# Optimization experiments

Measured on AMD Instinct MI355X. Metric: run time of the kernel, lower is better.

Reference implementation:

```python
import jax, jax.numpy as jnp
import numpy as np

B, L, H = 1024, 11, 128          # batch, seq_len-1 observations, cde_hidden_dim
VF, IF = 512, 256                # v_f_len, i_f_len
C = H + 1                        # control channels = time + reduced features
SUBSTEPS = 4                     # fixed RK4 substeps per eval interval (stand-in for solver step control)


def setup_inputs() -> dict:
    key = jax.random.key(0)
    ks = jax.random.split(key, 12)
    rn = lambda k, shape, s: jax.random.normal(k, shape, jnp.float32) * s
    F = VF + IF
    inp = {
        'fv': rn(ks[0], (B, L, VF), 1.0),
        'fi': rn(ks[1], (B, L, IF), 1.0),
        # strictly increasing timestamps
        'ts': jnp.cumsum(jax.random.uniform(ks[2], (B, L + 1), jnp.float32) * 0.1 + 0.01, axis=1),
        'w_red': rn(ks[3], (F, H), F ** -0.5), 'b_red': jnp.zeros((H,), jnp.float32),
        'w_init': rn(ks[4], (C, H), C ** -0.5), 'b_init': jnp.zeros((H,), jnp.float32),
        'w_h1': rn(ks[5], (H, H), H ** -0.5), 'b_h1': jnp.zeros((H,), jnp.float32),
        'w_h2': rn(ks[6], (H, H), H ** -0.5), 'b_h2': jnp.zeros((H,), jnp.float32),
        'w_out': rn(ks[7], (H, H * C), H ** -0.5), 'b_out': jnp.zeros((H * C,), jnp.float32),
        'w_r1': rn(ks[8], (H, 128), H ** -0.5), 'b_r1': jnp.zeros((128,), jnp.float32),
        'w_r2': rn(ks[9], (128, 6), 128 ** -0.5), 'b_r2': jnp.zeros((6,), jnp.float32),
    }
    return inp


def reference(fv, fi, ts, w_red, b_red, w_init, b_init, w_h1, b_h1, w_h2, b_h2,
              w_out, b_out, w_r1, b_r1, w_r2, b_r2):
    # fuse ('cat') + reduction_net
    fused = jnp.concatenate([fv, fi], axis=-1) @ w_red + b_red            # [B,L,H]
    tsd = (ts - ts[:, :1])[:, 1:, None]                                   # [B,L,1]
    x = jnp.concatenate([tsd, fused], axis=-1)                            # [B,L,C] control path; knots at t=0..L-1
    z0 = x[:, 0] @ w_init + b_init                                        # initial hidden state, [B,H]

    def field(z):                                                         # CDEFunc: [B,H] -> [B,H,C]
        h1 = jax.nn.relu(z @ w_h1 + b_h1)
        h2 = jax.nn.relu(h1 @ w_h2 + b_h2)
        return jnp.tanh(h2 @ w_out + b_out).reshape(-1, H, C)

    def dXdt(t):                                                          # piecewise-linear interpolation derivative
        idx = jnp.clip(jnp.floor(t).astype(jnp.int32), 0, L - 2)
        return x[:, idx + 1] - x[:, idx]                                  # [B,C]

    def vf(t, z):                                                         # dz/dt = f(z) @ dX/dt
        return jnp.einsum('bhc,bc->bh', field(z), dXdt(t))

    eval_times = jnp.linspace(0.1, 1.0, 10, dtype=jnp.float32)
    hstep = (eval_times[1] - eval_times[0]) / SUBSTEPS

    def rk4(z, t):
        k1 = vf(t, z)
        k2 = vf(t + hstep / 2, z + hstep / 2 * k1)
        k3 = vf(t + hstep / 2, z + hstep / 2 * k2)
        k4 = vf(t + hstep, z + hstep * k3)
        return z + hstep / 6 * (k1 + 2 * k2 + 2 * k3 + k4)

    def interval(z, t0):
        def body(zc, j):
            return rk4(zc, t0 + j * hstep), None
        z2, _ = jax.lax.scan(body, z, jnp.arange(SUBSTEPS, dtype=jnp.float32))
        return z2, z2

    _, zs = jax.lax.scan(interval, z0, eval_times[:-1])                   # [9,B,H]
    h_T = jnp.concatenate([z0[None], zs], axis=0).transpose(1, 0, 2)      # [B,10,H]

    a = h_T @ w_r1 + b_r1
    a = jnp.where(a > 0, a, 0.1 * a)                                      # LeakyReLU(0.1)
    poses = a @ w_r2 + b_r2                                               # [B,10,6]
    return poses, h_T[:, -1, :]
```

## Files before the change

### kernel.cpp

```cpp
#include <hip/hip_runtime.h>
#include <stdint.h>

typedef float   f32x4 __attribute__((ext_vector_type(4)));
typedef float   f32x2 __attribute__((ext_vector_type(2)));
typedef int     i32x4 __attribute__((ext_vector_type(4)));
typedef int     i32x2 __attribute__((ext_vector_type(2)));
typedef __bf16  bf16x8 __attribute__((ext_vector_type(8)));

#define DEV __device__ __forceinline__

DEV uint16_t f2bf(float f){
  uint32_t u = __float_as_uint(f);
  u += 0x7fffu + ((u >> 16) & 1u);
  return (uint16_t)(u >> 16);
}
DEV uint32_t pkbf(float lo, float hi){
  uint32_t r;
  asm("v_cvt_pk_bf16_f32 %0, %1, %2" : "=v"(r) : "v"(lo), "v"(hi));
  return r;
}
DEV uint32_t aoff(uint32_t row, uint32_t q){ return (row << 8) + (q ^ ((row & 7u) << 4)); }

DEV f32x4 MFMA(bf16x8 a, bf16x8 b, f32x4 c){
  return __builtin_amdgcn_mfma_f32_16x16x32_bf16(a, b, c, 0, 0, 0);
}

DEV uint64_t ld_ic64(const void* p){
  return __hip_atomic_load((const uint64_t*)p, __ATOMIC_RELAXED, __HIP_MEMORY_SCOPE_AGENT);
}
DEV uint32_t ld_ic32(const void* p){
  return __hip_atomic_load((const uint32_t*)p, __ATOMIC_RELAXED, __HIP_MEMORY_SCOPE_AGENT);
}
DEV void st_ic32(void* p, uint32_t v){
  __hip_atomic_store((uint32_t*)p, v, __ATOMIC_RELAXED, __HIP_MEMORY_SCOPE_AGENT);
}

DEV void bar_arrive(uint32_t* bar, uint32_t ep, int grp){
  uint32_t a = __hip_atomic_fetch_add(bar + grp*32, 1u, __ATOMIC_RELAXED, __HIP_MEMORY_SCOPE_AGENT);
  if (a == 32u*ep - 1u){
    uint32_t r = __hip_atomic_fetch_add(bar + 256, 1u, __ATOMIC_RELAXED, __HIP_MEMORY_SCOPE_AGENT);
    if (r == 8u*ep - 1u)
      __hip_atomic_store(bar + 288, ep, __ATOMIC_RELAXED, __HIP_MEMORY_SCOPE_AGENT);
  }
}
DEV void bar_wait(uint32_t* bar, uint32_t ep){
  int spins = 0;
  while (__hip_atomic_load(bar + 288, __ATOMIC_RELAXED, __HIP_MEMORY_SCOPE_AGENT) < ep){
    __builtin_amdgcn_s_sleep(1);
    if (++spins > (1 << 17)) break;
  }
  asm volatile("" ::: "memory");
}

__global__ __launch_bounds__(256) void pose_convT(const float* __restrict__ src,
    uint16_t* __restrict__ dst, int N, int MOD, int CB, float scale)
{
  __shared__ float tile[32][256];
  int bk = blockIdx.x & 3, bn = blockIdx.x >> 2;
  int k0 = bk * 32, n0 = bn * 256;
  int t = threadIdx.x;
  for (int r = 0; r < 32; r++){
    int n = n0 + t;
    tile[r][t] = (n < N) ? src[(size_t)(k0 + r) * N + n] : 0.f;
  }
  __syncthreads();
  int n = n0 + t;
  if (n < N){
    int c = n % MOD, h = n / MOD;
    #pragma unroll
    for (int o = 0; o < 4; o++){
      uint32_t w0 = (uint32_t)f2bf(tile[o*8+0][t]*scale) | ((uint32_t)f2bf(tile[o*8+1][t]*scale) << 16);
      uint32_t w1 = (uint32_t)f2bf(tile[o*8+2][t]*scale) | ((uint32_t)f2bf(tile[o*8+3][t]*scale) << 16);
      uint32_t w2 = (uint32_t)f2bf(tile[o*8+4][t]*scale) | ((uint32_t)f2bf(tile[o*8+5][t]*scale) << 16);
      uint32_t w3 = (uint32_t)f2bf(tile[o*8+6][t]*scale) | ((uint32_t)f2bf(tile[o*8+7][t]*scale) << 16);
      i32x4 val = { (int)w0, (int)w1, (int)w2, (int)w3 };
      uint32_t byte = (uint32_t)c * (uint32_t)CB + aoff((uint32_t)h, (uint32_t)(k0 + o*8) * 2);
      *(i32x4*)((char*)dst + byte) = val;
    }
  }
}

__global__ __launch_bounds__(256) void pose_misc(const float* __restrict__ b_out,
    const float* __restrict__ ts, float* __restrict__ bo_c, float* __restrict__ d0g)
{
  int i = blockIdx.x * 256 + threadIdx.x;
  if (i < 16512){
    int c = i % 129, h = i / 129;
    bo_c[c*128 + h] = b_out[i] * 2.8853900817779268f;
  }
  if (i < 1024) d0g[i] = ts[i*12 + 2] - ts[i*12 + 1];
}

__global__ __launch_bounds__(256) void pose_fused(
    const float* __restrict__ fv, const float* __restrict__ fi,
    const float* __restrict__ w_red, const float* __restrict__ b_red,
    float* __restrict__ F0, float* __restrict__ d0g)
{
  __shared__ float pk[128][16];
  __shared__ float res[16][128];
  const int b0 = blockIdx.x * 8;
  const int t = threadIdx.x;
  const int h = t & 127, sg = t >> 7;
  float acc[8] = {0.f,0.f,0.f,0.f,0.f,0.f,0.f,0.f};
  for (int p = 0; p < 6; p++){
    __syncthreads();
    { const int s  = t >> 4;
      const int ch = (t & 15) * 8;
      const int b  = b0 + (s & 7);
      const int ll = s >> 3;
      const int kb = p*128 + ch;
      const float* src = (kb < 512) ? (fv + ((size_t)b*11 + ll)*512 + kb)
                                    : (fi + ((size_t)b*11 + ll)*256 + (kb - 512));
      float v[8];
      #pragma unroll
      for (int j = 0; j < 8; j++) v[j] = src[j];
      #pragma unroll
      for (int j = 0; j < 8; j++) pk[ch + j][s] = v[j];
    }
    __syncthreads();
    #pragma unroll 4
    for (int kk = 0; kk < 128; kk++){
      const float wv = w_red[(size_t)(p*128 + kk)*128 + h];
      f32x4 v0 = *(const f32x4*)&pk[kk][sg*8];
      f32x4 v1 = *(const f32x4*)&pk[kk][sg*8 + 4];
      acc[0] += v0.x*wv; acc[1] += v0.y*wv; acc[2] += v0.z*wv; acc[3] += v0.w*wv;
      acc[4] += v1.x*wv; acc[5] += v1.y*wv; acc[6] += v1.z*wv; acc[7] += v1.w*wv;
    }
  }
  __syncthreads();
  const float br = b_red[h];
  #pragma unroll
  for (int si = 0; si < 8; si++) res[sg*8 + si][h] = acc[si] + br;
  __syncthreads();
  if (sg == 0){
    #pragma unroll
    for (int si = 0; si < 8; si++){
      const int b = b0 + si;
      const float f0 = res[si][h];
      const float f1 = res[8 + si][h];
      F0[(size_t)b*128 + h] = f0;
      d0g[(size_t)(1 + h)*1024 + b] = f1 - f0;
    }
  }
}

__global__ __launch_bounds__(512) void pose_init(
    const float* __restrict__ F0, const float* __restrict__ ts,
    const float* __restrict__ w_init, const float* __restrict__ b_init,
    const float* __restrict__ d0g,
    float* __restrict__ z_base, uint16_t* __restrict__ zbuf,
    float* __restrict__ hT, float* __restrict__ S)
{
  __shared__ float Ft[128][64];
  const int b0 = blockIdx.x * 64;
  const int t = threadIdx.x;
  { const int b = t >> 3, ch = (t & 7)*16;
    #pragma unroll
    for (int j = 0; j < 16; j++) Ft[ch + j][b] = F0[(size_t)(b0 + b)*128 + ch + j];
  }
  __syncthreads();
  const int h = t & 127, rg = t >> 7;
  float acc[16];
  const float w0 = w_init[h], bi = b_init[h];
  #pragma unroll
  for (int r = 0; r < 16; r++){
    const int b = b0 + rg*16 + r;
    acc[r] = (ts[b*12 + 1] - ts[b*12 + 0]) * w0 + bi;
  }
  #pragma unroll 2
  for (int j = 0; j < 128; j++){
    const float wv = w_init[(j + 1)*128 + h];
    const float* pr = &Ft[j][rg*16];
    #pragma unroll
    for (int q = 0; q < 4; q++){
      f32x4 v = *(const f32x4*)(pr + q*4);
      acc[q*4+0] += v.x*wv; acc[q*4+1] += v.y*wv; acc[q*4+2] += v.z*wv; acc[q*4+3] += v.w*wv;
    }
  }
  #pragma unroll
  for (int r = 0; r < 16; r++){
    const int b = b0 + rg*16 + r;
    const float z = acc[r];
    z_base[(size_t)b*128 + h] = z;
    hT[(size_t)b*1280 + h] = z;
    uint32_t byte = (uint32_t)(b >> 6) * 16384u + aoff((uint32_t)(b & 63), (uint32_t)h*2);
    *(uint16_t*)((char*)zbuf + byte) = f2bf(z);
  }
  if (t < 64){
    const int b = b0 + t;
    float s = 0.f;
    for (int c = 0; c < 129; c++) s += d0g[(size_t)c*1024 + b];
    S[b] = s;
  }
}

__global__ __launch_bounds__(512) void pose_persist(
    const uint16_t* __restrict__ Wt, const uint16_t* __restrict__ w1t,
    const uint16_t* __restrict__ w2t,
    const float* __restrict__ b1, const float* __restrict__ b2,
    const float* __restrict__ bo_c, const float* __restrict__ d0g,
    const float* __restrict__ Sv,
    uint16_t* __restrict__ zbuf, float* __restrict__ partials,
    const float* __restrict__ z_base,
    float* __restrict__ hT, uint32_t* __restrict__ bar)
{
  __shared__ uint16_t Yb[16384];
  __shared__ uint16_t Buf0[16384], Buf1[16384];
  __shared__ uint16_t H1[8192], H2[8192];
  __shared__ float    ztr[8][64];

  const int t   = threadIdx.x;
  const int blk = blockIdx.x;
  const int grp = blk & 7;
  const int mi  = blk >> 4;
  const int ci  = (blk & 7)*2 + ((blk >> 3) & 1);
  const int nc  = (ci == 15) ? 9 : 8;
  const int cbase = ci * 8;
  const int l  = t & 63, w = t >> 6;
  const int hh = w >> 2, bq = w & 3;
  const int l15 = l & 15, l4 = l >> 4;
  const int col16 = bq*16 + l15;
  const int bg = mi*64 + col16;

  const int h0B = (blk & 15) * 8;
  const int hB = h0B + (t >> 6), bB = mi*64 + (t & 63);
  const float HS = 0x1.999996p-6f;
  const float C2 = HS * 0.5f, C6 = HS / 6.f;
  float zb = z_base[(size_t)bB*128 + hB];
  float av = 0.f;
  const float Sb = Sv[bB];
  const char* zsl = (const char*)zbuf + (size_t)mi*16384;

  i32x4 Ra[4];
  auto ldst = [&](const void* g, i32x4* r){
    const i32x4* s = (const i32x4*)g;
    #pragma unroll
    for (int i = 0; i < 4; i++) r[i] = s[t + 512*i];
  };
  auto wrst = [&](uint16_t* lds, const i32x4* r){
    i32x4* d = (i32x4*)lds;
    #pragma unroll
    for (int i = 0; i < 4; i++) d[t + 512*i] = r[i];
  };
  auto chain_core = [&](const uint16_t* Wl, const bf16x8 (&bfr)[4], const float* bias, uint16_t* Dl){
    #pragma unroll
    for (int rt = 0; rt < 4; rt++){
      const int row = hh*64 + rt*16 + l15;
      bf16x8 afr[4];
      #pragma unroll
      for (int kb = 0; kb < 4; kb++)
        afr[kb] = *(const bf16x8*)((const char*)Wl + aoff((uint32_t)row, kb*64 + l4*16));
      const int h0 = hh*64 + rt*16 + l4*4;
      const f32x4 bias4 = *(const f32x4*)(bias + h0);
      f32x4 acc = {0.f,0.f,0.f,0.f};
      #pragma unroll
      for (int kb = 0; kb < 4; kb++) acc = MFMA(afr[kb], bfr[kb], acc);
      const float r0 = fmaxf(acc.x + bias4.x, 0.f);
      const float r1 = fmaxf(acc.y + bias4.y, 0.f);
      const float r2 = fmaxf(acc.z + bias4.z, 0.f);
      const float r3 = fmaxf(acc.w + bias4.w, 0.f);
      i32x2 pv = { (int)pkbf(r0, r1), (int)pkbf(r2, r3) };
      *(i32x2*)((char*)Dl + aoff((uint32_t)col16, (uint32_t)h0*2)) = pv;
    }
  };
  auto ld_bfr_lds = [&](const uint16_t* Bl, bf16x8 (&bfr)[4]){
    #pragma unroll
    for (int kb = 0; kb < 4; kb++)
      bfr[kb] = *(const bf16x8*)((const char*)Bl + aoff((uint32_t)col16, kb*64 + l4*16));
  };

  { i32x4 R0[4], R1[4], R2[4];
    ldst(w1t, R1); ldst(w2t, R2);
    ldst((const char*)Wt + (size_t)cbase*32768, R0);
    ldst((const char*)Wt + (size_t)(cbase + 1)*32768, Ra);
    wrst(Buf0, R1); wrst(Yb, R2); wrst(Buf1, R0);
  }
  __syncthreads();

  #pragma unroll 1
  for (int e = 0; e < 144; e++){
    bf16x8 bz[4];
    #pragma unroll
    for (int kb = 0; kb < 4; kb++){
      const char* a = zsl + aoff((uint32_t)col16, kb*64 + l4*16);
      union { uint64_t q[2]; bf16x8 v; } u;
      u.q[0] = ld_ic64(a);
      u.q[1] = ld_ic64(a + 8);
      bz[kb] = u.v;
    }
    chain_core(Buf0, bz, b1, H1);
    __syncthreads();
    { bf16x8 bh1[4];
      ld_bfr_lds(H1, bh1);
      chain_core(Yb, bh1, b2, H2);
    }
    __syncthreads();
    wrst(Buf0, Ra);

    bf16x8 bfr[4];
    ld_bfr_lds(H2, bfr);

    f32x4 out[4];
    const f32x4 Z4 = {0.f,0.f,0.f,0.f};
    #pragma unroll
    for (int rt = 0; rt < 4; rt++) out[rt] = Z4;

    for (int k = 0; k < nc; k++){
      const int c = cbase + k;
      const uint16_t* Wl = (k & 1) ? Buf0 : Buf1;
      if (k + 2 < nc) ldst((const char*)Wt + (size_t)(cbase + k + 2)*32768, Ra);
      const float d0 = d0g[(size_t)c*1024 + bg];
      #pragma unroll
      for (int rt = 0; rt < 4; rt++){
        const int row = hh*64 + rt*16 + l15;
        bf16x8 afr[4];
        #pragma unroll
        for (int kb = 0; kb < 4; kb++)
          afr[kb] = *(const bf16x8*)((const char*)Wl + aoff((uint32_t)row, kb*64 + l4*16));
        const int h0 = hh*64 + rt*16 + l4*4;
        const f32x4 bo4 = *(const f32x4*)(bo_c + c*128 + h0);
        f32x4 acc = {0.f,0.f,0.f,0.f};
        #pragma unroll
        for (int kb = 0; kb < 4; kb++) acc = MFMA(afr[kb], bfr[kb], acc);
        f32x4 rr;
        rr.x = __builtin_amdgcn_rcpf(__builtin_amdgcn_exp2f(acc.x + bo4.x) + 1.f);
        rr.y = __builtin_amdgcn_rcpf(__builtin_amdgcn_exp2f(acc.y + bo4.y) + 1.f);
        rr.z = __builtin_amdgcn_rcpf(__builtin_amdgcn_exp2f(acc.z + bo4.z) + 1.f);
        rr.w = __builtin_amdgcn_rcpf(__builtin_amdgcn_exp2f(acc.w + bo4.w) + 1.f);
        out[rt] += rr * d0;
      }
      __syncthreads();
      if (k + 2 < nc) wrst((k & 1) ? Buf0 : Buf1, Ra);
    }

    #pragma unroll
    for (int rt = 0; rt < 4; rt++){
      const int h0 = hh*64 + rt*16 + l4*4;
      #pragma unroll
      for (int j = 0; j < 4; j++){
        union { float f; uint32_t u; } v; v.f = out[rt][j];
        st_ic32(&partials[((size_t)ci*128 + h0 + j)*1024 + bg], v.u);
      }
    }
    __syncthreads();
    if (t == 0) bar_arrive(bar, (uint32_t)(2*e + 1), grp);

    if (e < 143){
      i32x4 R0[4], R1[4];
      ldst(w1t, R1);
      ldst((const char*)Wt + (size_t)cbase*32768, R0);
      ldst((const char*)Wt + (size_t)(cbase + 1)*32768, Ra);
      wrst(Buf0, R1); wrst(Buf1, R0);
    }
    if (t == 0) bar_wait(bar, (uint32_t)(2*e + 1));
    __syncthreads();

    {
      float s = 0.f;
      #pragma unroll
      for (int sl = 0; sl < 16; sl++){
        union { uint32_t u; float f; } v;
        v.u = ld_ic32(&partials[((size_t)sl*128 + hB)*1024 + bB]);
        s += v.f;
      }
      const float kk = Sb - 2.f*s;
      const int st = e & 3;
      float ze;
      if (st == 0){      av = kk;        ze = zb + C2*kk; }
      else if (st == 1){ av += 2.f*kk;   ze = zb + C2*kk; }
      else if (st == 2){ av += 2.f*kk;   ze = zb + HS*kk; }
      else {             zb += C6*(av + kk); ze = zb; }
      ztr[t >> 6][t & 63] = ze;
    }
    __syncthreads();
    if (t < 256){
      const int r = t >> 2, pp = t & 3;
      const uint32_t pv = pkbf(ztr[2*pp][r], ztr[2*pp + 1][r]);
      st_ic32((char*)zbuf + (size_t)mi*16384 + aoff((uint32_t)r, (uint32_t)(h0B + 2*pp)*2), pv);
    }
    if ((e & 15) == 15){
      const int r = t >> 3, hl = t & 7;
      hT[(size_t)(mi*64 + r)*1280 + (size_t)((e >> 4) + 1)*128 + h0B + hl] = ztr[hl][r];
    }
    __syncthreads();
    if (e < 143){
      if (t == 0){
        bar_arrive(bar, (uint32_t)(2*e + 2), grp);
        bar_wait(bar, (uint32_t)(2*e + 2));
      }
      __syncthreads();
    }
  }
}

__global__ __launch_bounds__(256) void pose_readout(
    const float* __restrict__ hT, const float* __restrict__ w_r1, const float* __restrict__ b_r1,
    const float* __restrict__ w_r2, const float* __restrict__ b_r2,
    float* __restrict__ out_poses, float* __restrict__ out_z)
{
  if (blockIdx.x >= 320){
    const int cb = blockIdx.x - 320;
    const int base = cb*2048 + threadIdx.x*4;
    #pragma unroll
    for (int p = 0; p < 2; p++){
      const int i = base + p*1024;
      const int b = i >> 7, h = i & 127;
      *(f32x4*)(out_z + i) = *(const f32x4*)(hT + (size_t)b*1280 + 1152 + h);
    }
    return;
  }
  __shared__ float htl[128][32];
  __shared__ float al[32][128];
  const int r0 = blockIdx.x * 32;
  const int t = threadIdx.x;
  { const int row = t >> 3, ch = (t & 7)*16;
    #pragma unroll
    for (int j = 0; j < 16; j++)
      htl[ch + j][row] = hT[(size_t)(r0 + row)*128 + ch + j];
  }
  __syncthreads();
  const int j = t & 127, rg = t >> 7;
  float a[16];
  const float bj = b_r1[j];
  #pragma unroll
  for (int r = 0; r < 16; r++) a[r] = bj;
  #pragma unroll 2
  for (int kk = 0; kk < 128; kk++){
    const float wv = w_r1[(size_t)kk*128 + j];
    const float* pr = &htl[kk][rg*16];
    #pragma unroll
    for (int q = 0; q < 4; q++){
      f32x4 v = *(const f32x4*)(pr + q*4);
      a[q*4+0] += v.x*wv; a[q*4+1] += v.y*wv; a[q*4+2] += v.z*wv; a[q*4+3] += v.w*wv;
    }
  }
  #pragma unroll
  for (int r = 0; r < 16; r++){
    float v = a[r];
    al[rg*16 + r][j] = (v > 0.f) ? v : 0.1f*v;
  }
  __syncthreads();
  if (t < 192){
    const int row = t / 6, p = t % 6;
    float s = b_r2[p];
    const float* ar = al[row];
    #pragma unroll 4
    for (int jj = 0; jj < 128; jj++) s += ar[jj] * w_r2[jj*6 + p];
    out_poses[(size_t)(r0 + row)*6 + p] = s;
  }
}

extern "C" void kernel_launch(void* const* d_in, const int* in_sizes, int n_in,
                              void* d_out, int out_size, void* d_ws, size_t ws_size,
                              hipStream_t stream)
{
  (void)in_sizes; (void)n_in; (void)out_size; (void)ws_size;
  const float* fv    = (const float*)d_in[0];
  const float* fi    = (const float*)d_in[1];
  const float* ts    = (const float*)d_in[2];
  const float* w_red = (const float*)d_in[3];
  const float* b_red = (const float*)d_in[4];
  const float* w_init= (const float*)d_in[5];
  const float* b_init= (const float*)d_in[6];
  const float* w_h1  = (const float*)d_in[7];
  const float* b_h1  = (const float*)d_in[8];
  const float* w_h2  = (const float*)d_in[9];
  const float* b_h2  = (const float*)d_in[10];
  const float* w_out = (const float*)d_in[11];
  const float* b_out = (const float*)d_in[12];
  const float* w_r1  = (const float*)d_in[13];
  const float* b_r1  = (const float*)d_in[14];
  const float* w_r2  = (const float*)d_in[15];
  const float* b_r2  = (const float*)d_in[16];

  char* p = (char*)d_ws;
  auto take = [&](size_t n){ char* r = p; p += (n + 255) & ~(size_t)255; return r; };
  uint32_t* bar   = (uint32_t*)take(4096);
  uint16_t* Wt    = (uint16_t*)take((size_t)129*32768);
  uint16_t* w1t   = (uint16_t*)take(32768);
  uint16_t* w2t   = (uint16_t*)take(32768);
  float* bo_c     = (float*)take((size_t)129*128*4);
  float* d0g      = (float*)take((size_t)129*1024*4);
  float* Sv       = (float*)take(1024*4);
  float* F0       = (float*)take((size_t)1024*128*4);
  float* z_base   = (float*)take((size_t)1024*128*4);
  uint16_t* zbuf  = (uint16_t*)take((size_t)16*16384);
  float* hT       = (float*)take((size_t)1024*10*128*4);
  float* partials = (float*)take((size_t)16*128*1024*4);

  float* out_poses = (float*)d_out;
  float* out_z     = (float*)d_out + 61440;

  const float SC = 2.8853900817779268f;

  hipMemsetAsync(bar, 0, 4096, stream);
  pose_convT<<<4,   256, 0, stream>>>(w_h1,  w1t, 128,   1,   0,     1.0f);
  pose_convT<<<4,   256, 0, stream>>>(w_h2,  w2t, 128,   1,   0,     1.0f);
  pose_convT<<<260, 256, 0, stream>>>(w_out, Wt,  16512, 129, 32768, SC);
  pose_misc <<<65,  256, 0, stream>>>(b_out, ts, bo_c, d0g);
  pose_fused<<<128, 256, 0, stream>>>(fv, fi, w_red, b_red, F0, d0g);
  pose_init <<<16,  512, 0, stream>>>(F0, ts, w_init, b_init, d0g, z_base, zbuf, hT, Sv);

  pose_persist<<<256, 512, 0, stream>>>(Wt, w1t, w2t, b_h1, b_h2, bo_c, d0g, Sv,
                                        zbuf, partials, z_base, hT, bar);

  pose_readout<<<384, 256, 0, stream>>>(hT, w_r1, b_r1, w_r2, b_r2, out_poses, out_z);
}
```

Baseline: 2.849 ms.

## Repartition persistent CDE kernel by hidden slice to keep W_out resident in LDS

The persistent kernel now splits work as 8 batch tiles by 32 hidden-output slices. Each block keeps its full 128KB slice of the output weight resident in LDS instead of streaming control-channel chunks from global memory every step. The cross-block reduction through a global partials buffer and one of the two grid barriers per step are removed, since each block now reduces over all channels locally. z is double-buffered in global memory in an MFMA fragment layout. The cost is that the small h1/h2 MLP is recomputed redundantly in every hidden-slice block, and LDS use rises to about 160KB.

```diff
diff --git a/kernel.cpp b/kernel.cpp
--- a/kernel.cpp
+++ b/kernel.cpp
@@ -24,15 +24,13 @@
 DEV f32x4 MFMA(bf16x8 a, bf16x8 b, f32x4 c){
   return __builtin_amdgcn_mfma_f32_16x16x32_bf16(a, b, c, 0, 0, 0);
 }
+DEV bf16x8 as_bf(i32x4 v){ union { i32x4 i; bf16x8 b; } u; u.i = v; return u.b; }
 
 DEV uint64_t ld_ic64(const void* p){
   return __hip_atomic_load((const uint64_t*)p, __ATOMIC_RELAXED, __HIP_MEMORY_SCOPE_AGENT);
 }
-DEV uint32_t ld_ic32(const void* p){
-  return __hip_atomic_load((const uint32_t*)p, __ATOMIC_RELAXED, __HIP_MEMORY_SCOPE_AGENT);
-}
-DEV void st_ic32(void* p, uint32_t v){
-  __hip_atomic_store((uint32_t*)p, v, __ATOMIC_RELAXED, __HIP_MEMORY_SCOPE_AGENT);
+DEV void st_ic64(void* p, uint64_t v){
+  __hip_atomic_store((uint64_t*)p, v, __ATOMIC_RELAXED, __HIP_MEMORY_SCOPE_AGENT);
 }
 
 DEV void bar_arrive(uint32_t* bar, uint32_t ep, int grp){
@@ -47,54 +45,84 @@
   int spins = 0;
   while (__hip_atomic_load(bar + 288, __ATOMIC_RELAXED, __HIP_MEMORY_SCOPE_AGENT) < ep){
     __builtin_amdgcn_s_sleep(1);
-    if (++spins > (1 << 17)) break;
+    if (++spins > (1 << 20)) break;
   }
   asm volatile("" ::: "memory");
 }
 
-__global__ __launch_bounds__(256) void pose_convT(const float* __restrict__ src,
-    uint16_t* __restrict__ dst, int N, int MOD, int CB, float scale)
+__global__ __launch_bounds__(256) void pose_convW(const float* __restrict__ src,
+    uint16_t* __restrict__ Wg, uint16_t* __restrict__ w0f)
 {
   __shared__ float tile[32][256];
+  const float SC = 2.8853900817779268f;
   int bk = blockIdx.x & 3, bn = blockIdx.x >> 2;
   int k0 = bk * 32, n0 = bn * 256;
   int t = threadIdx.x;
   for (int r = 0; r < 32; r++){
     int n = n0 + t;
-    tile[r][t] = (n < N) ? src[(size_t)(k0 + r) * N + n] : 0.f;
+    tile[r][t] = (n < 16512) ? src[(size_t)(k0 + r) * 16512 + n] : 0.f;
   }
   __syncthreads();
   int n = n0 + t;
-  if (n < N){
-    int c = n % MOD, h = n / MOD;
+  if (n < 16512){
+    int c = n % 129, hfull = n / 129;
+    int ht = hfull >> 2;
     #pragma unroll
     for (int o = 0; o < 4; o++){
-      uint32_t w0 = (uint32_t)f2bf(tile[o*8+0][t]*scale) | ((uint32_t)f2bf(tile[o*8+1][t]*scale) << 16);
-      uint32_t w1 = (uint32_t)f2bf(tile[o*8+2][t]*scale) | ((uint32_t)f2bf(tile[o*8+3][t]*scale) << 16);
-      uint32_t w2 = (uint32_t)f2bf(tile[o*8+4][t]*scale) | ((uint32_t)f2bf(tile[o*8+5][t]*scale) << 16);
-      uint32_t w3 = (uint32_t)f2bf(tile[o*8+6][t]*scale) | ((uint32_t)f2bf(tile[o*8+7][t]*scale) << 16);
+      uint32_t w0 = (uint32_t)f2bf(tile[o*8+0][t]*SC) | ((uint32_t)f2bf(tile[o*8+1][t]*SC) << 16);
+      uint32_t w1 = (uint32_t)f2bf(tile[o*8+2][t]*SC) | ((uint32_t)f2bf(tile[o*8+3][t]*SC) << 16);
+      uint32_t w2 = (uint32_t)f2bf(tile[o*8+4][t]*SC) | ((uint32_t)f2bf(tile[o*8+5][t]*SC) << 16);
+      uint32_t w3 = (uint32_t)f2bf(tile[o*8+6][t]*SC) | ((uint32_t)f2bf(tile[o*8+7][t]*SC) << 16);
       i32x4 val = { (int)w0, (int)w1, (int)w2, (int)w3 };
-      uint32_t byte = (uint32_t)c * (uint32_t)CB + aoff((uint32_t)h, (uint32_t)(k0 + o*8) * 2);
-      *(i32x4*)((char*)dst + byte) = val;
-    }
+      uint32_t kg = (uint32_t)(k0 + o*8);
+      if (c > 0){
+        uint32_t r = (uint32_t)(c - 1)*4 + (hfull & 3);
+        uint32_t byte = (uint32_t)ht*131072u + r*256u + ((kg*2u) ^ ((r & 7u) << 4));
+        *(i32x4*)((char*)Wg + byte) = val;
+      } else {
+        uint32_t r0 = (uint32_t)(hfull & 3);
+        uint32_t byte = (uint32_t)ht*4096u + (kg >> 5)*1024u + (r0 + 16u*((kg >> 3) & 3u))*16u;
+        *(i32x4*)((char*)w0f + byte) = val;
+      }
+    }
+  }
+}
+
+__global__ __launch_bounds__(256) void pose_convC(const float* __restrict__ w_h1,
+    const float* __restrict__ w_h2, uint32_t* __restrict__ w1f, uint32_t* __restrict__ w2f)
+{
+  const float* src = blockIdx.x ? w_h2 : w_h1;
+  uint32_t* dst = blockIdx.x ? w2f : w1f;
+  int t = threadIdx.x;
+  for (int ii = 0; ii < 32; ii++){
+    int u = t*32 + ii;
+    int p = u & 3, l = (u >> 2) & 63, kb = (u >> 8) & 3, Mt = u >> 10;
+    int k = kb*32 + (l >> 4)*8 + 2*p;
+    int n = Mt*16 + (l & 15);
+    uint32_t v = (uint32_t)f2bf(src[(size_t)k*128 + n]) |
+                 ((uint32_t)f2bf(src[(size_t)(k+1)*128 + n]) << 16);
+    dst[u] = v;
   }
 }
 
 __global__ __launch_bounds__(256) void pose_misc(const float* __restrict__ b_out,
-    const float* __restrict__ ts, float* __restrict__ bo_c, float* __restrict__ d0g)
-{
+    const float* __restrict__ ts, float* __restrict__ bo_f, float* __restrict__ bo_t,
+    float* __restrict__ d0t)
+{
+  const float SC = 2.8853900817779268f;
   int i = blockIdx.x * 256 + threadIdx.x;
   if (i < 16512){
     int c = i % 129, h = i / 129;
-    bo_c[c*128 + h] = b_out[i] * 2.8853900817779268f;
-  }
-  if (i < 1024) d0g[i] = ts[i*12 + 2] - ts[i*12 + 1];
+    if (c == 0) bo_t[h] = b_out[i] * SC;
+    else        bo_f[(size_t)(c-1)*128 + h] = b_out[i] * SC;
+  }
+  if (i < 1024) d0t[i] = ts[i*12 + 2] - ts[i*12 + 1];
 }
 
 __global__ __launch_bounds__(256) void pose_fused(
     const float* __restrict__ fv, const float* __restrict__ fi,
     const float* __restrict__ w_red, const float* __restrict__ b_red,
-    float* __restrict__ F0, float* __restrict__ d0g)
+    float* __restrict__ F0, float* __restrict__ d0f)
 {
   __shared__ float pk[128][16];
   __shared__ float res[16][128];
@@ -139,16 +167,21 @@
       const float f0 = res[si][h];
       const float f1 = res[8 + si][h];
       F0[(size_t)b*128 + h] = f0;
-      d0g[(size_t)(1 + h)*1024 + b] = f1 - f0;
-    }
-  }
+      d0f[(size_t)h*1024 + b] = f1 - f0;
+    }
+  }
+}
+
+DEV uint32_t zaddr(int b, int h){
+  return (uint32_t)(b >> 7)*32768u + (uint32_t)((b >> 4) & 7)*4096u + (uint32_t)(h >> 5)*1024u
+       + ((uint32_t)(b & 15) + 16u*(((uint32_t)h & 31u) >> 3))*16u + ((uint32_t)h & 7u)*2u;
 }
 
 __global__ __launch_bounds__(512) void pose_init(
     const float* __restrict__ F0, const float* __restrict__ ts,
     const float* __restrict__ w_init, const float* __restrict__ b_init,
-    const float* __restrict__ d0g,
-    float* __restrict__ z_base, uint16_t* __restrict__ zbuf,
+    const float* __restrict__ d0f, const float* __restrict__ d0t,
+    float* __restrict__ z_base, uint16_t* __restrict__ zfG,
     float* __restrict__ hT, float* __restrict__ S)
 {
   __shared__ float Ft[128][64];
@@ -183,210 +216,238 @@
     const float z = acc[r];
     z_base[(size_t)b*128 + h] = z;
     hT[(size_t)b*1280 + h] = z;
-    uint32_t byte = (uint32_t)(b >> 6) * 16384u + aoff((uint32_t)(b & 63), (uint32_t)h*2);
-    *(uint16_t*)((char*)zbuf + byte) = f2bf(z);
+    *(uint16_t*)((char*)zfG + zaddr(b, h)) = f2bf(z);
   }
   if (t < 64){
     const int b = b0 + t;
-    float s = 0.f;
-    for (int c = 0; c < 129; c++) s += d0g[(size_t)c*1024 + b];
+    float s = d0t[b];
+    for (int j = 0; j < 128; j++) s += d0f[(size_t)j*1024 + b];
     S[b] = s;
   }
 }
 
-__global__ __launch_bounds__(512) void pose_persist(
-    const uint16_t* __restrict__ Wt, const uint16_t* __restrict__ w1t,
-    const uint16_t* __restrict__ w2t,
+__global__ __launch_bounds__(512, 2) void pose_persist(
+    const uint16_t* __restrict__ Wg, const uint32_t* __restrict__ w1f,
+    const uint32_t* __restrict__ w2f, const uint16_t* __restrict__ w0f,
     const float* __restrict__ b1, const float* __restrict__ b2,
-    const float* __restrict__ bo_c, const float* __restrict__ d0g,
-    const float* __restrict__ Sv,
-    uint16_t* __restrict__ zbuf, float* __restrict__ partials,
-    const float* __restrict__ z_base,
-    float* __restrict__ hT, uint32_t* __restrict__ bar)
-{
-  __shared__ uint16_t Yb[16384];
-  __shared__ uint16_t Buf0[16384], Buf1[16384];
-  __shared__ uint16_t H1[8192], H2[8192];
-  __shared__ float    ztr[8][64];
-
+    const float* __restrict__ bo_f, const float* __restrict__ bo_t,
+    const float* __restrict__ d0f, const float* __restrict__ d0t,
+    const float* __restrict__ Sv, const float* __restrict__ z_base,
+    uint16_t* __restrict__ zfG, float* __restrict__ hT, uint32_t* __restrict__ bar)
+{
+  __shared__ __align__(16) char Lds[163840];
+  const uint32_t HB = 131072u;
   const int t   = threadIdx.x;
   const int blk = blockIdx.x;
+  const int bt  = blk & 7;
+  const int ht  = blk >> 3;
   const int grp = blk & 7;
-  const int mi  = blk >> 4;
-  const int ci  = (blk & 7)*2 + ((blk >> 3) & 1);
-  const int nc  = (ci == 15) ? 9 : 8;
-  const int cbase = ci * 8;
-  const int l  = t & 63, w = t >> 6;
-  const int hh = w >> 2, bq = w & 3;
-  const int l15 = l & 15, l4 = l >> 4;
-  const int col16 = bq*16 + l15;
-  const int bg = mi*64 + col16;
-
-  const int h0B = (blk & 15) * 8;
-  const int hB = h0B + (t >> 6), bB = mi*64 + (t & 63);
+  const int w   = t >> 6, l = t & 63;
+  const int l15 = l & 15, l4g = l >> 4;
+  const int mw  = w >> 1, nw = w & 1;
+
+  { const i32x4* src = (const i32x4*)((const char*)Wg + (size_t)ht*131072);
+    i32x4* dst = (i32x4*)Lds;
+    #pragma unroll
+    for (int i = 0; i < 16; i++) dst[t + 512*i] = src[t + 512*i];
+  }
+
+  bf16x8 w1A[4];
+  #pragma unroll
+  for (int kb = 0; kb < 4; kb++)
+    w1A[kb] = as_bf(*(const i32x4*)((const char*)w1f + (size_t)(w*4 + kb)*1024 + l*16));
+
+  float d0M[8][4];
+  #pragma unroll
+  for (int i = 0; i < 8; i++)
+    #pragma unroll
+    for (int nt = 0; nt < 4; nt++)
+      d0M[i][nt] = d0f[(size_t)((mw*8 + i)*4 + l4g)*1024 + bt*128 + nw*64 + nt*16 + l15];
+  float d0c0[4];
+  #pragma unroll
+  for (int nt = 0; nt < 4; nt++)
+    d0c0[nt] = (l4g == 0) ? d0t[bt*128 + nw*64 + nt*16 + l15] : 0.f;
+
+  const int bl = t >> 2, hp = t & 3;
+  const int bB = bt*128 + bl, hB = ht*4 + hp;
   const float HS = 0x1.999996p-6f;
   const float C2 = HS * 0.5f, C6 = HS / 6.f;
   float zb = z_base[(size_t)bB*128 + hB];
   float av = 0.f;
   const float Sb = Sv[bB];
-  const char* zsl = (const char*)zbuf + (size_t)mi*16384;
-
-  i32x4 Ra[4];
-  auto ldst = [&](const void* g, i32x4* r){
-    const i32x4* s = (const i32x4*)g;
-    #pragma unroll
-    for (int i = 0; i < 4; i++) r[i] = s[t + 512*i];
-  };
-  auto wrst = [&](uint16_t* lds, const i32x4* r){
-    i32x4* d = (i32x4*)lds;
-    #pragma unroll
-    for (int i = 0; i < 4; i++) d[t + 512*i] = r[i];
-  };
-  auto chain_core = [&](const uint16_t* Wl, const bf16x8 (&bfr)[4], const float* bias, uint16_t* Dl){
-    #pragma unroll
-    for (int rt = 0; rt < 4; rt++){
-      const int row = hh*64 + rt*16 + l15;
-      bf16x8 afr[4];
-      #pragma unroll
-      for (int kb = 0; kb < 4; kb++)
-        afr[kb] = *(const bf16x8*)((const char*)Wl + aoff((uint32_t)row, kb*64 + l4*16));
-      const int h0 = hh*64 + rt*16 + l4*4;
-      const f32x4 bias4 = *(const f32x4*)(bias + h0);
-      f32x4 acc = {0.f,0.f,0.f,0.f};
-      #pragma unroll
-      for (int kb = 0; kb < 4; kb++) acc = MFMA(afr[kb], bfr[kb], acc);
-      const float r0 = fmaxf(acc.x + bias4.x, 0.f);
-      const float r1 = fmaxf(acc.y + bias4.y, 0.f);
-      const float r2 = fmaxf(acc.z + bias4.z, 0.f);
-      const float r3 = fmaxf(acc.w + bias4.w, 0.f);
-      i32x2 pv = { (int)pkbf(r0, r1), (int)pkbf(r2, r3) };
-      *(i32x2*)((char*)Dl + aoff((uint32_t)col16, (uint32_t)h0*2)) = pv;
-    }
-  };
-  auto ld_bfr_lds = [&](const uint16_t* Bl, bf16x8 (&bfr)[4]){
-    #pragma unroll
-    for (int kb = 0; kb < 4; kb++)
-      bfr[kb] = *(const bf16x8*)((const char*)Bl + aoff((uint32_t)col16, kb*64 + l4*16));
-  };
-
-  { i32x4 R0[4], R1[4], R2[4];
-    ldst(w1t, R1); ldst(w2t, R2);
-    ldst((const char*)Wt + (size_t)cbase*32768, R0);
-    ldst((const char*)Wt + (size_t)(cbase + 1)*32768, Ra);
-    wrst(Buf0, R1); wrst(Yb, R2); wrst(Buf1, R0);
-  }
+
+  const uint32_t zsl_off = (uint32_t)bt*32768u;
   __syncthreads();
 
   #pragma unroll 1
   for (int e = 0; e < 144; e++){
-    bf16x8 bz[4];
-    #pragma unroll
-    for (int kb = 0; kb < 4; kb++){
-      const char* a = zsl + aoff((uint32_t)col16, kb*64 + l4*16);
-      union { uint64_t q[2]; bf16x8 v; } u;
-      u.q[0] = ld_ic64(a);
-      u.q[1] = ld_ic64(a + 8);
-      bz[kb] = u.v;
-    }
-    chain_core(Buf0, bz, b1, H1);
-    __syncthreads();
-    { bf16x8 bh1[4];
-      ld_bfr_lds(H1, bh1);
-      chain_core(Yb, bh1, b2, H2);
-    }
-    __syncthreads();
-    wrst(Buf0, Ra);
-
-    bf16x8 bfr[4];
-    ld_bfr_lds(H2, bfr);
-
-    f32x4 out[4];
-    const f32x4 Z4 = {0.f,0.f,0.f,0.f};
-    #pragma unroll
-    for (int rt = 0; rt < 4; rt++) out[rt] = Z4;
-
-    for (int k = 0; k < nc; k++){
-      const int c = cbase + k;
-      const uint16_t* Wl = (k & 1) ? Buf0 : Buf1;
-      if (k + 2 < nc) ldst((const char*)Wt + (size_t)(cbase + k + 2)*32768, Ra);
-      const float d0 = d0g[(size_t)c*1024 + bg];
-      #pragma unroll
-      for (int rt = 0; rt < 4; rt++){
-        const int row = hh*64 + rt*16 + l15;
-        bf16x8 afr[4];
+    const char* zsrc = (const char*)zfG + (size_t)(e & 1)*262144 + zsl_off;
+    #pragma unroll
+    for (int i = 0; i < 4; i++){
+      union { uint64_t q[2]; i32x4 v; } u;
+      u.q[0] = ld_ic64(zsrc + t*16 + i*8192);
+      u.q[1] = ld_ic64(zsrc + t*16 + i*8192 + 8);
+      *(i32x4*)(Lds + HB + t*16 + i*8192) = u.v;
+    }
+    __syncthreads();
+
+    const f32x4 b1v = *(const f32x4*)(b1 + w*16 + l4g*4);
+    #pragma unroll
+    for (int hh = 0; hh < 2; hh++){
+      bf16x8 bz[4][4];
+      #pragma unroll
+      for (int nt2 = 0; nt2 < 4; nt2++){
+        const int Nt = hh*4 + nt2;
         #pragma unroll
         for (int kb = 0; kb < 4; kb++)
-          afr[kb] = *(const bf16x8*)((const char*)Wl + aoff((uint32_t)row, kb*64 + l4*16));
-        const int h0 = hh*64 + rt*16 + l4*4;
-        const f32x4 bo4 = *(const f32x4*)(bo_c + c*128 + h0);
+          bz[nt2][kb] = as_bf(*(const i32x4*)(Lds + HB + Nt*4096 + kb*1024 + l*16));
+      }
+      __syncthreads();
+      #pragma unroll
+      for (int nt2 = 0; nt2 < 4; nt2++){
         f32x4 acc = {0.f,0.f,0.f,0.f};
         #pragma unroll
-        for (int kb = 0; kb < 4; kb++) acc = MFMA(afr[kb], bfr[kb], acc);
+        for (int kb = 0; kb < 4; kb++) acc = MFMA(w1A[kb], bz[nt2][kb], acc);
+        const int col = (hh*4 + nt2)*16 + l15;
+        const float r0 = fmaxf(acc.x + b1v.x, 0.f);
+        const float r1 = fmaxf(acc.y + b1v.y, 0.f);
+        const float r2 = fmaxf(acc.z + b1v.z, 0.f);
+        const float r3 = fmaxf(acc.w + b1v.w, 0.f);
+        i32x2 pv = { (int)pkbf(r0, r1), (int)pkbf(r2, r3) };
+        *(i32x2*)(Lds + HB + aoff((uint32_t)col, (uint32_t)(w*16 + l4g*4)*2)) = pv;
+      }
+      __syncthreads();
+    }
+
+    { bf16x8 bh1[4];
+      #pragma unroll
+      for (int kb = 0; kb < 4; kb++)
+        bh1[kb] = as_bf(*(const i32x4*)(Lds + HB + aoff((uint32_t)(w*16 + l15), kb*64 + l4g*16)));
+      #pragma unroll
+      for (int Mt = 0; Mt < 8; Mt++){
+        bf16x8 a2[4];
+        #pragma unroll
+        for (int kb = 0; kb < 4; kb++)
+          a2[kb] = as_bf(*(const i32x4*)((const char*)w2f + (size_t)(Mt*4 + kb)*1024 + l*16));
+        f32x4 acc = {0.f,0.f,0.f,0.f};
+        #pragma unroll
+        for (int kb = 0; kb < 4; kb++) acc = MFMA(a2[kb], bh1[kb], acc);
+        const f32x4 b2v = *(const f32x4*)(b2 + Mt*16 + l4g*4);
+        const float r0 = fmaxf(acc.x + b2v.x, 0.f);
+        const float r1 = fmaxf(acc.y + b2v.y, 0.f);
+        const float r2 = fmaxf(acc.z + b2v.z, 0.f);
+        const float r3 = fmaxf(acc.w + b2v.w, 0.f);
+        i32x2 pv = { (int)pkbf(r0, r1), (int)pkbf(r2, r3) };
+        *(i32x2*)(Lds + HB + aoff((uint32_t)(w*16 + l15), (uint32_t)(Mt*16 + l4g*4)*2)) = pv;
+      }
+    }
+    __syncthreads();
+
+    bf16x8 bh2[4][4];
+    #pragma unroll
+    for (int nt = 0; nt < 4; nt++)
+      #pragma unroll
+      for (int kb = 0; kb < 4; kb++)
+        bh2[nt][kb] = as_bf(*(const i32x4*)(Lds + HB + aoff((uint32_t)(nw*64 + nt*16 + l15), kb*64 + l4g*16)));
+    __syncthreads();
+
+    f32x4 oacc[4];
+    const f32x4 Z4 = {0.f,0.f,0.f,0.f};
+    #pragma unroll
+    for (int nt = 0; nt < 4; nt++) oacc[nt] = Z4;
+
+    #pragma unroll 2
+    for (int i = 0; i < 8; i++){
+      const int Mt = mw*8 + i;
+      bf16x8 A[4];
+      #pragma unroll
+      for (int kb = 0; kb < 4; kb++)
+        A[kb] = as_bf(*(const i32x4*)(Lds + aoff((uint32_t)(Mt*16 + l15), kb*64 + l4g*16)));
+      const f32x4 bo4 = *(const f32x4*)(bo_f + (size_t)(Mt*4 + l4g)*128 + ht*4);
+      #pragma unroll
+      for (int nt = 0; nt < 4; nt++){
+        f32x4 acc = {0.f,0.f,0.f,0.f};
+        #pragma unroll
+        for (int kb = 0; kb < 4; kb++) acc = MFMA(A[kb], bh2[nt][kb], acc);
         f32x4 rr;
         rr.x = __builtin_amdgcn_rcpf(__builtin_amdgcn_exp2f(acc.x + bo4.x) + 1.f);
         rr.y = __builtin_amdgcn_rcpf(__builtin_amdgcn_exp2f(acc.y + bo4.y) + 1.f);
         rr.z = __builtin_amdgcn_rcpf(__builtin_amdgcn_exp2f(acc.z + bo4.z) + 1.f);
         rr.w = __builtin_amdgcn_rcpf(__builtin_amdgcn_exp2f(acc.w + bo4.w) + 1.f);
-        out[rt] += rr * d0;
-      }
-      __syncthreads();
-      if (k + 2 < nc) wrst((k & 1) ? Buf0 : Buf1, Ra);
-    }
-
-    #pragma unroll
-    for (int rt = 0; rt < 4; rt++){
-      const int h0 = hh*64 + rt*16 + l4*4;
-      #pragma unroll
-      for (int j = 0; j < 4; j++){
-        union { float f; uint32_t u; } v; v.f = out[rt][j];
-        st_ic32(&partials[((size_t)ci*128 + h0 + j)*1024 + bg], v.u);
-      }
-    }
-    __syncthreads();
-    if (t == 0) bar_arrive(bar, (uint32_t)(2*e + 1), grp);
-
-    if (e < 143){
-      i32x4 R0[4], R1[4];
-      ldst(w1t, R1);
-      ldst((const char*)Wt + (size_t)cbase*32768, R0);
-      ldst((const char*)Wt + (size_t)(cbase + 1)*32768, Ra);
-      wrst(Buf0, R1); wrst(Buf1, R0);
-    }
-    if (t == 0) bar_wait(bar, (uint32_t)(2*e + 1));
+        oacc[nt] += rr * d0M[i][nt];
+      }
+    }
+    if (mw == 0){
+      bf16x8 A0[4];
+      #pragma unroll
+      for (int kb = 0; kb < 4; kb++)
+        A0[kb] = as_bf(*(const i32x4*)((const char*)w0f + (size_t)ht*4096 + kb*1024 + l*16));
+      const f32x4 bt4 = *(const f32x4*)(bo_t + ht*4);
+      #pragma unroll
+      for (int nt = 0; nt < 4; nt++){
+        f32x4 acc = {0.f,0.f,0.f,0.f};
+        #pragma unroll
+        for (int kb = 0; kb < 4; kb++) acc = MFMA(A0[kb], bh2[nt][kb], acc);
+        f32x4 rr;
+        rr.x = __builtin_amdgcn_rcpf(__builtin_amdgcn_exp2f(acc.x + bt4.x) + 1.f);
+        rr.y = __builtin_amdgcn_rcpf(__builtin_amdgcn_exp2f(acc.y + bt4.y) + 1.f);
+        rr.z = __builtin_amdgcn_rcpf(__builtin_amdgcn_exp2f(acc.z + bt4.z) + 1.f);
+        rr.w = __builtin_amdgcn_rcpf(__builtin_amdgcn_exp2f(acc.w + bt4.w) + 1.f);
+        oacc[nt] += rr * d0c0[nt];
+      }
+    }
+
+    #pragma unroll
+    for (int nt = 0; nt < 4; nt++){
+      #pragma unroll
+      for (int c = 0; c < 4; c++){
+        float v = oacc[nt][c];
+        v += __shfl_xor(v, 16, 64);
+        v += __shfl_xor(v, 32, 64);
+        oacc[nt][c] = v;
+      }
+    }
+    if (l < 16){
+      #pragma unroll
+      for (int nt = 0; nt < 4; nt++){
+        const int b = nw*64 + nt*16 + l15;
+        *(f32x4*)(Lds + HB + mw*2048 + b*16) = oacc[nt];
+      }
+    }
     __syncthreads();
 
     {
-      float s = 0.f;
-      #pragma unroll
-      for (int sl = 0; sl < 16; sl++){
-        union { uint32_t u; float f; } v;
-        v.u = ld_ic32(&partials[((size_t)sl*128 + hB)*1024 + bB]);
-        s += v.f;
-      }
-      const float kk = Sb - 2.f*s;
+      float p = 0.f;
+      #pragma unroll
+      for (int m = 0; m < 4; m++)
+        p += *(const float*)(Lds + HB + m*2048 + bl*16 + hp*4);
+      const float kk = Sb - 2.f*p;
       const int st = e & 3;
       float ze;
       if (st == 0){      av = kk;        ze = zb + C2*kk; }
       else if (st == 1){ av += 2.f*kk;   ze = zb + C2*kk; }
       else if (st == 2){ av += 2.f*kk;   ze = zb + HS*kk; }
-      else {             zb += C6*(av + kk); ze = zb; }
-      ztr[t >> 6][t & 63] = ze;
-    }
-    __syncthreads();
-    if (t < 256){
-      const int r = t >> 2, pp = t & 3;
-      const uint32_t pv = pkbf(ztr[2*pp][r], ztr[2*pp + 1][r]);
-      st_ic32((char*)zbuf + (size_t)mi*16384 + aoff((uint32_t)r, (uint32_t)(h0B + 2*pp)*2), pv);
-    }
-    if ((e & 15) == 15){
-      const int r = t >> 3, hl = t & 7;
-      hT[(size_t)(mi*64 + r)*1280 + (size_t)((e >> 4) + 1)*128 + h0B + hl] = ztr[hl][r];
+      else {
+        zb += C6*(av + kk); ze = zb;
+        if ((e & 15) == 15)
+          hT[(size_t)bB*1280 + (size_t)((e >> 4) + 1)*128 + hB] = zb;
+      }
+      *(uint16_t*)(Lds + HB + 8192 + t*2) = f2bf(ze);
+    }
+    __syncthreads();
+
+    if (t < 128){
+      uint64_t zw = *(const uint64_t*)(Lds + HB + 8192 + t*8);
+      char* zdst = (char*)zfG + (size_t)((e + 1) & 1)*262144 + zsl_off
+                 + (t >> 4)*4096 + (ht >> 3)*1024
+                 + ((t & 15) + 16*((ht & 7) >> 1))*16 + (ht & 1)*8;
+      st_ic64(zdst, zw);
     }
     __syncthreads();
     if (e < 143){
       if (t == 0){
-        bar_arrive(bar, (uint32_t)(2*e + 2), grp);
-        bar_wait(bar, (uint32_t)(2*e + 2));
+        bar_arrive(bar, (uint32_t)(e + 1), grp);
+        bar_wait(bar, (uint32_t)(e + 1));
       }
       __syncthreads();
     }
@@ -476,33 +537,33 @@
   char* p = (char*)d_ws;
   auto take = [&](size_t n){ char* r = p; p += (n + 255) & ~(size_t)255; return r; };
   uint32_t* bar   = (uint32_t*)take(4096);
-  uint16_t* Wt    = (uint16_t*)take((size_t)129*32768);
-  uint16_t* w1t   = (uint16_t*)take(32768);
-  uint16_t* w2t   = (uint16_t*)take(32768);
-  float* bo_c     = (float*)take((size_t)129*128*4);
-  float* d0g      = (float*)take((size_t)129*1024*4);
+  uint16_t* Wg    = (uint16_t*)take((size_t)32*131072);
+  uint16_t* w0f   = (uint16_t*)take((size_t)32*4096);
+  uint32_t* w1f   = (uint32_t*)take(32768);
+  uint32_t* w2f   = (uint32_t*)take(32768);
+  float* bo_f     = (float*)take((size_t)128*128*4);
+  float* bo_t     = (float*)take(128*4);
+  float* d0f      = (float*)take((size_t)128*1024*4);
+  float* d0t      = (float*)take(1024*4);
   float* Sv       = (float*)take(1024*4);
   float* F0       = (float*)take((size_t)1024*128*4);
   float* z_base   = (float*)take((size_t)1024*128*4);
-  uint16_t* zbuf  = (uint16_t*)take((size_t)16*16384);
+  uint16_t* zfG   = (uint16_t*)take((size_t)2*262144);
   float* hT       = (float*)take((size_t)1024*10*128*4);
-  float* partials = (float*)take((size_t)16*128*1024*4);
 
   float* out_poses = (float*)d_out;
   float* out_z     = (float*)d_out + 61440;
 
-  const float SC = 2.8853900817779268f;
-
   hipMemsetAsync(bar, 0, 4096, stream);
-  pose_convT<<<4,   256, 0, stream>>>(w_h1,  w1t, 128,   1,   0,     1.0f);
-  pose_convT<<<4,   256, 0, stream>>>(w_h2,  w2t, 128,   1,   0,     1.0f);
-  pose_convT<<<260, 256, 0, stream>>>(w_out, Wt,  16512, 129, 32768, SC);
-  pose_misc <<<65,  256, 0, stream>>>(b_out, ts, bo_c, d0g);
-  pose_fused<<<128, 256, 0, stream>>>(fv, fi, w_red, b_red, F0, d0g);
-  pose_init <<<16,  512, 0, stream>>>(F0, ts, w_init, b_init, d0g, z_base, zbuf, hT, Sv);
-
-  pose_persist<<<256, 512, 0, stream>>>(Wt, w1t, w2t, b_h1, b_h2, bo_c, d0g, Sv,
-                                        zbuf, partials, z_base, hT, bar);
+  hipMemsetAsync(w0f, 0, (size_t)32*4096*2, stream);
+  pose_convW<<<260, 256, 0, stream>>>(w_out, Wg, w0f);
+  pose_convC<<<2,   256, 0, stream>>>(w_h1, w_h2, w1f, w2f);
+  pose_misc <<<65,  256, 0, stream>>>(b_out, ts, bo_f, bo_t, d0t);
+  pose_fused<<<128, 256, 0, stream>>>(fv, fi, w_red, b_red, F0, d0f);
+  pose_init <<<16,  512, 0, stream>>>(F0, ts, w_init, b_init, d0f, d0t, z_base, zfG, hT, Sv);
+
+  pose_persist<<<256, 512, 0, stream>>>(Wg, w1f, w2f, w0f, b_h1, b_h2, bo_f, bo_t,
+                                        d0f, d0t, Sv, z_base, zfG, hT, bar);
 
   pose_readout<<<384, 256, 0, stream>>>(hT, w_r1, b_r1, w_r2, b_r2, out_poses, out_z);
 }
```

Measured after the change: 3.403 ms. 1.19x slower.
